# Performance work log

Measured on AMD Instinct MI355X. Metric: run time of the kernel, lower is better.

## Reference

```python
import jax, jax.numpy as jnp
import numpy as np
from jax.scipy.special import logsumexp

SINKHORN_ALPHA = 20.0
OT_MAX_ITER = 100
STOP_THR = 0.005


def setup_inputs() -> dict:
    key = jax.random.key(0)
    k1, k2 = jax.random.split(key)
    x = jax.random.normal(k1, (256, 384), dtype=jnp.float32)   # topic embeddings [K, D]
    y = jax.random.normal(k2, (32768, 384), dtype=jnp.float32)  # word embeddings  [V, D]
    return {"x": x, "y": y}


def reference(x, y):
    n, m = x.shape[0], y.shape[0]
    # FASTopic pairwise_euclidean_distance: squared euclidean cost [n, m]
    M = jnp.sum(x * x, axis=1, keepdims=True) + jnp.sum(y * y, axis=1) - 2.0 * (x @ y.T)
    a = jnp.full((n, 1), 1.0 / n, dtype=M.dtype)
    b = jnp.full((m, 1), 1.0 / m, dtype=M.dtype)
    log_a = jnp.log(a + 1e-30)
    log_b = jnp.log(b + 1e-30)
    log_K0 = -M * SINKHORN_ALPHA

    # State trick: the original mutates log_K only at the periodic absorption step
    # (log_K += log_u + log_v.T). We keep log_K = log_K0 + cum_u + cum_v.T so the
    # carried state is only O(n + m) vectors; math is identical.
    def body(state):
        log_u, log_v, cum_u, cum_v, err, cpt = state
        log_K = log_K0 + cum_u + cum_v.T                                    # [n, m]
        log_v_n = log_b - logsumexp(log_K.T + log_u.T, axis=1)[:, None]     # [m, 1]
        log_u_n = log_a - logsumexp(log_K + log_v_n.T, axis=1)[:, None]     # [n, 1]
        cpt_n = cpt + 1

        def absorb(_):
            cu = cum_u + log_u_n
            cv = cum_v + log_v_n
            lK = log_K0 + cu + cv.T
            # marginal check with log_u = log_v = 0 (matches check_convergence)
            row = jnp.exp(logsumexp(lK, axis=1))[:, None]
            col = jnp.exp(logsumexp(lK, axis=0))[:, None]
            e = jnp.maximum(jnp.max(jnp.abs(row - a)), jnp.max(jnp.abs(col - b)))
            return jnp.zeros_like(log_u_n), jnp.zeros_like(log_v_n), cu, cv, e

        def keep(_):
            return log_u_n, log_v_n, cum_u, cum_v, err

        lu, lv, cu, cv, e = jax.lax.cond(cpt_n % 50 == 1, absorb, keep, None)
        return (lu, lv, cu, cv, e, cpt_n)

    def cond_fn(state):
        err, cpt = state[4], state[5]
        return (err > STOP_THR) & (cpt < OT_MAX_ITER)

    init = (jnp.zeros((n, 1), M.dtype), jnp.zeros((m, 1), M.dtype),
            jnp.zeros((n, 1), M.dtype), jnp.zeros((m, 1), M.dtype),
            jnp.array(1.0, M.dtype), jnp.array(0, jnp.int32))
    log_u, log_v, cum_u, cum_v, _, _ = jax.lax.while_loop(cond_fn, body, init)

    log_K = log_K0 + cum_u + cum_v.T
    transp = jnp.exp(log_u) * (jnp.exp(log_K) * jnp.exp(log_v).T)  # diag(u) K diag(v)
    loss_ETP = jnp.sum(transp * M)
    return loss_ETP, transp
```

## Files before the change

### kernel.cpp

```cpp
#include <hip/hip_runtime.h>
#include <math.h>


#define N_TOPIC 256
#define N_WORD  32768

static constexpr float LOG_A = -5.545177444479562f;
static constexpr float LOG_B = -10.397207708399179f;
static constexpr float BVAL  = 3.0517578125e-05f;

typedef float f32x4 __attribute__((ext_vector_type(4)));
typedef short bf16x8 __attribute__((ext_vector_type(8)));

#define PIN4(v) asm volatile("" : "+v"((v).x), "+v"((v).y), "+v"((v).z), "+v"((v).w))

__global__ __launch_bounds__(256) void init_k(
    const float* __restrict__ x, const float* __restrict__ y,
    float* __restrict__ nx, float* __restrict__ ny, float* __restrict__ su,
    unsigned* __restrict__ colerr, int* __restrict__ active,
    int* __restrict__ counters, float* __restrict__ out)
{
    const int b = blockIdx.x, t = threadIdx.x;
    const int w = t >> 6, l = t & 63;
    if (b < 8192) {
        const int r = (b << 2) + w;
        const float4* y4 = (const float4*)y;
        float4 v = y4[r * 96 + l];
        float s = v.x * v.x + v.y * v.y + v.z * v.z + v.w * v.w;
        if (l < 32) {
            float4 u = y4[r * 96 + 64 + l];
            s += u.x * u.x + u.y * u.y + u.z * u.z + u.w * u.w;
        }
        for (int off = 32; off; off >>= 1) s += __shfl_down(s, off);
        if (l == 0) ny[r] = s;
    } else if (b < 8256) {
        const int r = ((b - 8192) << 2) + w;
        const float4* x4 = (const float4*)x;
        float4 v = x4[r * 96 + l];
        float s = v.x * v.x + v.y * v.y + v.z * v.z + v.w * v.w;
        if (l < 32) {
            float4 u = x4[r * 96 + 64 + l];
            s += u.x * u.x + u.y * u.y + u.z * u.z + u.w * u.w;
        }
        for (int off = 32; off; off >>= 1) s += __shfl_down(s, off);
        if (l == 0) { nx[r] = s; su[r] = -20.f * s; }
    } else {
        for (int k = t; k < 4096; k += 256) counters[k] = 0;
        if (t == 0) { colerr[0] = 0u; colerr[1] = 0u; active[0] = 1; out[0] = 0.f; }
    }
}

static __device__ __forceinline__ void split3(float v, ushort& h0, ushort& h1, ushort& h2)
{
    unsigned u0 = __float_as_uint(v);
    h0 = (ushort)(u0 >> 16);
    float r1 = v - __uint_as_float(u0 & 0xFFFF0000u);
    unsigned u1 = __float_as_uint(r1);
    h1 = (ushort)(u1 >> 16);
    float r2 = r1 - __uint_as_float(u1 & 0xFFFF0000u);
    h2 = (ushort)(__float_as_uint(r2) >> 16);
}

__global__ __launch_bounds__(256, 1) void gemm_k(
    const float* __restrict__ x, const float* __restrict__ y, float* __restrict__ G)
{
    __shared__ __align__(16) ushort xs0[5120], xs1[5120], xs2[5120];
    __shared__ __align__(16) ushort ys0[5120], ys1[5120], ys2[5120];

    const int t   = threadIdx.x;
    const int jb  = blockIdx.x << 7;
    const int ib  = blockIdx.y << 7;
    const int w   = t >> 6;
    const int ln  = t & 63;
    const int q   = ln >> 4;
    const int l15 = ln & 15;

    const float4* x4 = (const float4*)x;
    const float4* y4 = (const float4*)y;

    f32x4 acc[2][8];
#pragma unroll
    for (int mi = 0; mi < 2; ++mi)
#pragma unroll
        for (int nj = 0; nj < 8; ++nj) acc[mi][nj] = (f32x4){0.f, 0.f, 0.f, 0.f};

    for (int kc = 0; kc < 12; ++kc) {
        __syncthreads();
#pragma unroll
        for (int p = 0; p < 4; ++p) {
            const int f  = (t << 2) + p;
            const int r  = f >> 3, c4 = f & 7;
            const int o  = r * 40 + (c4 << 2);
            float4 vx = x4[(ib + r) * 96 + (kc << 3) + c4];
            ushort a0,a1,a2,b0,b1,b2,c0,c1,c2,d0,d1,d2;
            split3(vx.x, a0,a1,a2); split3(vx.y, b0,b1,b2);
            split3(vx.z, c0,c1,c2); split3(vx.w, d0,d1,d2);
            *(ushort4*)&xs0[o] = make_ushort4(a0,b0,c0,d0);
            *(ushort4*)&xs1[o] = make_ushort4(a1,b1,c1,d1);
            *(ushort4*)&xs2[o] = make_ushort4(a2,b2,c2,d2);
            float4 vy = y4[(jb + r) * 96 + (kc << 3) + c4];
            split3(vy.x, a0,a1,a2); split3(vy.y, b0,b1,b2);
            split3(vy.z, c0,c1,c2); split3(vy.w, d0,d1,d2);
            *(ushort4*)&ys0[o] = make_ushort4(a0,b0,c0,d0);
            *(ushort4*)&ys1[o] = make_ushort4(a1,b1,c1,d1);
            *(ushort4*)&ys2[o] = make_ushort4(a2,b2,c2,d2);
        }
        __syncthreads();

        bf16x8 A[3][2];
#pragma unroll
        for (int mi = 0; mi < 2; ++mi) {
            const int off = ((w << 5) + (mi << 4) + l15) * 40 + (q << 3);
            A[0][mi] = *(const bf16x8*)&xs0[off];
            A[1][mi] = *(const bf16x8*)&xs1[off];
            A[2][mi] = *(const bf16x8*)&xs2[off];
        }
#pragma unroll
        for (int nj = 0; nj < 8; ++nj) {
            const int off = ((nj << 4) + l15) * 40 + (q << 3);
            bf16x8 B0 = *(const bf16x8*)&ys0[off];
            bf16x8 B1 = *(const bf16x8*)&ys1[off];
            bf16x8 B2 = *(const bf16x8*)&ys2[off];
#pragma unroll
            for (int mi = 0; mi < 2; ++mi) {
                f32x4 c = acc[mi][nj];
                c = __builtin_amdgcn_mfma_f32_16x16x32_bf16(A[0][mi], B0, c, 0, 0, 0);
                c = __builtin_amdgcn_mfma_f32_16x16x32_bf16(A[0][mi], B1, c, 0, 0, 0);
                c = __builtin_amdgcn_mfma_f32_16x16x32_bf16(A[1][mi], B0, c, 0, 0, 0);
                c = __builtin_amdgcn_mfma_f32_16x16x32_bf16(A[1][mi], B1, c, 0, 0, 0);
                c = __builtin_amdgcn_mfma_f32_16x16x32_bf16(A[0][mi], B2, c, 0, 0, 0);
                c = __builtin_amdgcn_mfma_f32_16x16x32_bf16(A[2][mi], B0, c, 0, 0, 0);
                acc[mi][nj] = c;
            }
        }
    }
#pragma unroll
    for (int mi = 0; mi < 2; ++mi) {
        const int gi0 = ib + (w << 5) + (mi << 4) + (q << 2);
#pragma unroll
        for (int nj = 0; nj < 8; ++nj) {
            float* base = &G[(size_t)blockIdx.x * 32768 + (size_t)gi0 * 128
                             + (nj << 4) + l15];
#pragma unroll
            for (int r = 0; r < 4; ++r)
                base[r * 128] = 40.f * acc[mi][nj][r];
        }
    }
}

static __device__ __forceinline__ bool bar_arrive(int* cnt, int ph, int t, int* lastf)
{
    __threadfence();
    if (t == 0) *lastf = (atomicAdd(&cnt[ph], 1) == 255);
    __syncthreads();
    return *lastf != 0;
}
static __device__ __forceinline__ void bar_release(int* gen, int ph, int t)
{
    __threadfence();
    if (t == 0) atomicExch(gen, ph);
}
static __device__ __forceinline__ void bar_wait(int* gen, int ph, int t)
{
    if (t == 0) {
        while (atomicCAS(gen, -1, -1) < ph) __builtin_amdgcn_s_sleep(2);
    }
    __syncthreads();
    __threadfence();
}

__global__ __launch_bounds__(256, 1) void sink_loop(
    const float* __restrict__ G, float* __restrict__ su,
    float* __restrict__ W, float2* __restrict__ pms, float* __restrict__ prow,
    int* __restrict__ cnt, int* __restrict__ gen,
    unsigned* __restrict__ colerr, int* __restrict__ active)
{
    __shared__ float su_lds[256];
    __shared__ float mm[1024];
    __shared__ float ss[1024];
    __shared__ float Mcol[128];
    __shared__ float Wlds[128];
    __shared__ float ecol[128];
    __shared__ float Rlds[256];
    __shared__ float pq[256 * 33];
    __shared__ float errb[128];
    __shared__ int lastf;

    const int t  = threadIdx.x;
    const int b  = blockIdx.x;
    const int jq = t & 31;
    const int ig = t >> 5;
    const int c0 = jq << 2;
    int ph = 1;

    const float4* G4 = (const float4*)G;
    float4 tile[32];
#pragma unroll
    for (int k = 0; k < 32; ++k) {
        const int i = ig + (k << 3);
        tile[k] = G4[((size_t)b << 13) + (i << 5) + jq];
    }
#pragma unroll
    for (int k = 0; k < 32; ++k) PIN4(tile[k]);

    su_lds[t] = su[t];
    __syncthreads();

    {
        float m0=-INFINITY,m1=-INFINITY,m2=-INFINITY,m3=-INFINITY;
#pragma unroll
        for (int k = 0; k < 32; ++k) {
            const float sk = su_lds[ig + (k << 3)];
            m0=fmaxf(m0,tile[k].x+sk); m1=fmaxf(m1,tile[k].y+sk);
            m2=fmaxf(m2,tile[k].z+sk); m3=fmaxf(m3,tile[k].w+sk);
        }
        float s0=0.f,s1=0.f,s2=0.f,s3=0.f;
#pragma unroll
        for (int k = 0; k < 32; ++k) {
            const float sk = su_lds[ig + (k << 3)];
            s0+=__expf(tile[k].x+sk-m0); s1+=__expf(tile[k].y+sk-m1);
            s2+=__expf(tile[k].z+sk-m2); s3+=__expf(tile[k].w+sk-m3);
        }
        mm[ig*128+c0+0]=m0; ss[ig*128+c0+0]=s0;
        mm[ig*128+c0+1]=m1; ss[ig*128+c0+1]=s1;
        mm[ig*128+c0+2]=m2; ss[ig*128+c0+2]=s2;
        mm[ig*128+c0+3]=m3; ss[ig*128+c0+3]=s3;
        __syncthreads();
        if (t < 128) {
            float m=-INFINITY, s=0.f;
#pragma unroll
            for (int q = 0; q < 8; ++q) {
                float pmv=mm[q*128+t], psv=ss[q*128+t];
                float nm=fmaxf(m,pmv);
                s = s*__expf(m-nm) + psv*__expf(pmv-nm);
                m = nm;
            }
            Wlds[t] = LOG_B - (m + __logf(s));
        }
        __syncthreads();
    }
    {
#pragma unroll
        for (int k = 0; k < 32; ++k) {
            const int i = ig + (k << 3);
            float a0=tile[k].x+Wlds[c0], a1=tile[k].y+Wlds[c0+1];
            float a2=tile[k].z+Wlds[c0+2], a3=tile[k].w+Wlds[c0+3];
            pq[i*33+jq] = fmaxf(fmaxf(a0,a1), fmaxf(a2,a3));
        }
        __syncthreads();
        {
            float R=-INFINITY;
#pragma unroll
            for (int q = 0; q < 32; ++q) R = fmaxf(R, pq[t*33+q]);
            Rlds[t] = R;
        }
        __syncthreads();
#pragma unroll
        for (int k = 0; k < 32; ++k) {
            const int i = ig + (k << 3);
            const float Rr = Rlds[i];
            float s = __expf(tile[k].x+Wlds[c0]-Rr)   + __expf(tile[k].y+Wlds[c0+1]-Rr)
                    + __expf(tile[k].z+Wlds[c0+2]-Rr) + __expf(tile[k].w+Wlds[c0+3]-Rr);
            pq[i*33+jq] = s;
        }
        __syncthreads();
        {
            float s = 0.f;
#pragma unroll
            for (int q = 0; q < 32; ++q) s += pq[t*33+q];
            pms[(b << 8) + t] = make_float2(Rlds[t], s);
        }
    }
    if (bar_arrive(cnt, ph, t, &lastf)) {
        __threadfence();
        float m=-INFINITY, s=0.f;
        for (int p = 0; p < 256; ++p) {
            float2 v = pms[(p << 8) + t];
            float nm = fmaxf(m, v.x);
            s = s*__expf(m-nm) + v.y*__expf(v.x-nm);
            m = nm;
        }
        su[t] = LOG_A - (m + __logf(s));
        bar_release(gen, ph, t);
    }
    bar_wait(gen, ph, t); ++ph;
    su_lds[t] = su[t];
    __syncthreads();

    int act;
    {
        float m0=-INFINITY,m1=-INFINITY,m2=-INFINITY,m3=-INFINITY;
#pragma unroll
        for (int k = 0; k < 32; ++k) {
            const float sk = su_lds[ig + (k << 3)];
            m0=fmaxf(m0,tile[k].x+sk); m1=fmaxf(m1,tile[k].y+sk);
            m2=fmaxf(m2,tile[k].z+sk); m3=fmaxf(m3,tile[k].w+sk);
        }
        float s0=0.f,s1=0.f,s2=0.f,s3=0.f;
#pragma unroll
        for (int k = 0; k < 32; ++k) {
            const float sk = su_lds[ig + (k << 3)];
            s0+=__expf(tile[k].x+sk-m0); s1+=__expf(tile[k].y+sk-m1);
            s2+=__expf(tile[k].z+sk-m2); s3+=__expf(tile[k].w+sk-m3);
        }
        mm[ig*128+c0+0]=m0; ss[ig*128+c0+0]=s0;
        mm[ig*128+c0+1]=m1; ss[ig*128+c0+1]=s1;
        mm[ig*128+c0+2]=m2; ss[ig*128+c0+2]=s2;
        mm[ig*128+c0+3]=m3; ss[ig*128+c0+3]=s3;
        __syncthreads();
        float d = 0.f;
        if (t < 128) {
            float m=-INFINITY, s=0.f;
#pragma unroll
            for (int q = 0; q < 8; ++q) {
                float pmv=mm[q*128+t], psv=ss[q*128+t];
                float nm=fmaxf(m,pmv);
                s = s*__expf(m-nm) + psv*__expf(pmv-nm);
                m = nm;
            }
            d = fabsf(__expf((m + __logf(s)) + Wlds[t]) - BVAL);
            errb[t] = d;
        }
        __syncthreads();
        for (int n = 64; n; n >>= 1) {
            if (t < n) errb[t] = fmaxf(errb[t], errb[t + n]);
            __syncthreads();
        }
        if (t == 0) atomicMax(&colerr[0], __float_as_uint(errb[0]));
        if (bar_arrive(cnt, ph, t, &lastf)) {
            if (t == 0) {
                unsigned e = atomicMax(&colerr[0], 0u);
                active[0] = (__uint_as_float(e) > 0.005f) ? 1 : 0;
            }
            bar_release(gen, ph, t);
        }
        bar_wait(gen, ph, t); ++ph;
        act = active[0];
    }

    if (act) {
#pragma unroll 1
        for (int tt = 2; tt <= 100; ++tt) {
            {
                float m0=-INFINITY,m1=-INFINITY,m2=-INFINITY,m3=-INFINITY;
#pragma unroll
                for (int k = 0; k < 32; ++k) {
                    const float sk = su_lds[ig + (k << 3)];
                    m0=fmaxf(m0,tile[k].x+sk); m1=fmaxf(m1,tile[k].y+sk);
                    m2=fmaxf(m2,tile[k].z+sk); m3=fmaxf(m3,tile[k].w+sk);
                }
                mm[ig*128+c0+0]=m0; mm[ig*128+c0+1]=m1;
                mm[ig*128+c0+2]=m2; mm[ig*128+c0+3]=m3;
                __syncthreads();
                if (t < 128) {
                    float m=-INFINITY;
#pragma unroll
                    for (int q = 0; q < 8; ++q) m = fmaxf(m, mm[q*128+t]);
                    Mcol[t] = m;
                }
                __syncthreads();
            }
            float4 E[32];
            {
                const float Mc0=Mcol[c0], Mc1=Mcol[c0+1], Mc2=Mcol[c0+2], Mc3=Mcol[c0+3];
                float s0=0.f,s1=0.f,s2=0.f,s3=0.f;
#pragma unroll
                for (int k = 0; k < 32; ++k) {
                    const float sk = su_lds[ig + (k << 3)];
                    E[k].x=__expf(tile[k].x+sk-Mc0); s0+=E[k].x;
                    E[k].y=__expf(tile[k].y+sk-Mc1); s1+=E[k].y;
                    E[k].z=__expf(tile[k].z+sk-Mc2); s2+=E[k].z;
                    E[k].w=__expf(tile[k].w+sk-Mc3); s3+=E[k].w;
                }
                ss[ig*128+c0+0]=s0; ss[ig*128+c0+1]=s1;
                ss[ig*128+c0+2]=s2; ss[ig*128+c0+3]=s3;
                __syncthreads();
                if (t < 128) {
                    float ssum = 0.f;
#pragma unroll
                    for (int q = 0; q < 8; ++q) ssum += ss[q*128+t];
                    Wlds[t] = LOG_B - (Mcol[t] + __logf(ssum));
                    ecol[t] = 1.0f / ssum;
                }
                __syncthreads();
            }
            {
                const float e0=ecol[c0], e1=ecol[c0+1], e2=ecol[c0+2], e3=ecol[c0+3];
#pragma unroll
                for (int k = 0; k < 32; ++k) {
                    const int i = ig + (k << 3);
                    pq[i*33+jq] = E[k].x*e0 + E[k].y*e1 + E[k].z*e2 + E[k].w*e3;
                }
                __syncthreads();
                float s = 0.f;
#pragma unroll
                for (int q = 0; q < 32; ++q) s += pq[t*33+q];
                prow[(b << 8) + t] = s;
            }
            if (bar_arrive(cnt, ph, t, &lastf)) {
                __threadfence();
                float tot = 0.f;
                for (int p = 0; p < 256; ++p) tot += prow[(p << 8) + t];
                su[t] = (LOG_A - LOG_B) + su_lds[t] - __logf(tot);
                bar_release(gen, ph, t);
            }
            bar_wait(gen, ph, t); ++ph;
            su_lds[t] = su[t];
            __syncthreads();

            if (tt == 51) {
                float m0=-INFINITY,m1=-INFINITY,m2=-INFINITY,m3=-INFINITY;
#pragma unroll
                for (int k = 0; k < 32; ++k) {
                    const float sk = su_lds[ig + (k << 3)];
                    m0=fmaxf(m0,tile[k].x+sk); m1=fmaxf(m1,tile[k].y+sk);
                    m2=fmaxf(m2,tile[k].z+sk); m3=fmaxf(m3,tile[k].w+sk);
                }
                float s0=0.f,s1=0.f,s2=0.f,s3=0.f;
#pragma unroll
                for (int k = 0; k < 32; ++k) {
                    const float sk = su_lds[ig + (k << 3)];
                    s0+=__expf(tile[k].x+sk-m0); s1+=__expf(tile[k].y+sk-m1);
                    s2+=__expf(tile[k].z+sk-m2); s3+=__expf(tile[k].w+sk-m3);
                }
                mm[ig*128+c0+0]=m0; ss[ig*128+c0+0]=s0;
                mm[ig*128+c0+1]=m1; ss[ig*128+c0+1]=s1;
                mm[ig*128+c0+2]=m2; ss[ig*128+c0+2]=s2;
                mm[ig*128+c0+3]=m3; ss[ig*128+c0+3]=s3;
                __syncthreads();
                if (t < 128) {
                    float m=-INFINITY, s=0.f;
#pragma unroll
                    for (int q = 0; q < 8; ++q) {
                        float pmv=mm[q*128+t], psv=ss[q*128+t];
                        float nm=fmaxf(m,pmv);
                        s = s*__expf(m-nm) + psv*__expf(pmv-nm);
                        m = nm;
                    }
                    errb[t] = fabsf(__expf((m + __logf(s)) + Wlds[t]) - BVAL);
                }
                __syncthreads();
                for (int n = 64; n; n >>= 1) {
                    if (t < n) errb[t] = fmaxf(errb[t], errb[t + n]);
                    __syncthreads();
                }
                if (t == 0) atomicMax(&colerr[1], __float_as_uint(errb[0]));
                if (bar_arrive(cnt, ph, t, &lastf)) {
                    if (t == 0) {
                        unsigned e = atomicMax(&colerr[1], 0u);
                        active[0] = (__uint_as_float(e) > 0.005f) ? 1 : 0;
                    }
                    bar_release(gen, ph, t);
                }
                bar_wait(gen, ph, t); ++ph;
                if (active[0] == 0) break;
            }
        }
    }

    if (t < 128) W[(b << 7) + t] = Wlds[t];
}

__global__ __launch_bounds__(256) void finalize_k(
    const float* __restrict__ G, const float* __restrict__ su,
    const float* __restrict__ W, const float* __restrict__ nx,
    const float* __restrict__ ny, float* __restrict__ out)
{
    __shared__ float su_lds[256], nx_lds[256];
    __shared__ float red[4];
    const int t = threadIdx.x, b = blockIdx.x;
    const int j0 = b << 7;
    const int jq = t & 31;
    const int ig = t >> 5;
    su_lds[t] = su[t];
    nx_lds[t] = nx[t];
    __syncthreads();

    const float4* G4 = (const float4*)G;
    const float4 Wq  = ((const float4*)W)[(j0 >> 2) + jq];
    const float4 nyq = ((const float4*)ny)[(j0 >> 2) + jq];
    const int jbase = 1 + j0 + (jq << 2);
    float acc = 0.f;
#pragma unroll 4
    for (int it = 0; it < 32; ++it) {
        const int i = ig + (it << 3);
        float4 g = G4[((size_t)b << 13) + (i << 5) + jq];
        const float si = su_lds[i], nxi = nx_lds[i];
        float v0 = __expf(g.x + si + Wq.x);
        float v1 = __expf(g.y + si + Wq.y);
        float v2 = __expf(g.z + si + Wq.z);
        float v3 = __expf(g.w + si + Wq.w);
        float* o = out + jbase + (size_t)i * 32768;
        __builtin_nontemporal_store(v0, o + 0);
        __builtin_nontemporal_store(v1, o + 1);
        __builtin_nontemporal_store(v2, o + 2);
        __builtin_nontemporal_store(v3, o + 3);
        acc += v0 * (nxi + nyq.x - 0.05f * g.x) +
               v1 * (nxi + nyq.y - 0.05f * g.y) +
               v2 * (nxi + nyq.z - 0.05f * g.z) +
               v3 * (nxi + nyq.w - 0.05f * g.w);
    }
    for (int off = 32; off; off >>= 1) acc += __shfl_down(acc, off);
    if ((t & 63) == 0) red[t >> 6] = acc;
    __syncthreads();
    if (t == 0) atomicAdd(out, red[0] + red[1] + red[2] + red[3]);
}

extern "C" void kernel_launch(void* const* d_in, const int* in_sizes, int n_in,
                              void* d_out, int out_size, void* d_ws, size_t ws_size,
                              hipStream_t stream)
{
    const float* x = (const float*)d_in[0];
    const float* y = (const float*)d_in[1];
    float* out = (float*)d_out;

    float* ws   = (float*)d_ws;
    float* G    = ws;
    float* Wv   = G + 8388608;
    float* su   = Wv + 32768;
    float* nx   = su + 256;
    float* ny   = nx + 256;
    float2* pms = (float2*)(ny + 32768);
    float* prow = (float*)(pms + 65536);
    unsigned* colerr = (unsigned*)(prow + 65536);
    int* active   = (int*)(colerr + 2);
    int* counters = active + 1;
    int* gen      = counters + 3000;

    init_k<<<8257, 256, 0, stream>>>(x, y, nx, ny, su, colerr, active, counters, out);
    gemm_k<<<dim3(256, 2), 256, 0, stream>>>(x, y, G);
    sink_loop<<<256, 256, 0, stream>>>(G, su, Wv, pms, prow,
                                       counters, gen, colerr, active);
    finalize_k<<<256, 256, 0, stream>>>(G, su, Wv, nx, ny, out);
}
```

Baseline: 308.2 us.

## Fuse GEMM, Sinkhorn loop and finalize into one persistent kernel

Merges the GEMM, the persistent Sinkhorn loop and the finalize kernel into a single 256-block kernel. Each block computes its own 256x128 cost tile in MFMA registers, moves it into the register tile through LDS, and reuses that tile for the final transport-plan output. This removes the 32 MB G write and its two reads, plus two kernel launches. In exchange each block now does the whole GEMM for its column strip (x split into bf16 parts per block, 4x8 accumulators), which means only 256 blocks run the GEMM and register pressure rises.

```diff
diff --git a/kernel.cpp b/kernel.cpp
--- a/kernel.cpp
+++ b/kernel.cpp
@@ -61,59 +61,110 @@
     h2 = (ushort)(__float_as_uint(r2) >> 16);
 }
 
-__global__ __launch_bounds__(256, 1) void gemm_k(
-    const float* __restrict__ x, const float* __restrict__ y, float* __restrict__ G)
-{
-    __shared__ __align__(16) ushort xs0[5120], xs1[5120], xs2[5120];
-    __shared__ __align__(16) ushort ys0[5120], ys1[5120], ys2[5120];
-
-    const int t   = threadIdx.x;
-    const int jb  = blockIdx.x << 7;
-    const int ib  = blockIdx.y << 7;
-    const int w   = t >> 6;
-    const int ln  = t & 63;
-    const int q   = ln >> 4;
-    const int l15 = ln & 15;
+static __device__ __forceinline__ bool bar_arrive(int* cnt, int ph, int t, int* lastf)
+{
+    __threadfence();
+    if (t == 0) *lastf = (atomicAdd(&cnt[ph], 1) == 255);
+    __syncthreads();
+    return *lastf != 0;
+}
+static __device__ __forceinline__ void bar_release(int* gen, int ph, int t)
+{
+    __threadfence();
+    if (t == 0) atomicExch(gen, ph);
+}
+static __device__ __forceinline__ void bar_wait(int* gen, int ph, int t)
+{
+    if (t == 0) {
+        while (atomicCAS(gen, -1, -1) < ph) __builtin_amdgcn_s_sleep(2);
+    }
+    __syncthreads();
+    __threadfence();
+}
+
+__global__ __launch_bounds__(256, 1) void fused_k(
+    const float* __restrict__ x, const float* __restrict__ y,
+    float* __restrict__ su, const float* __restrict__ nx,
+    const float* __restrict__ ny, float2* __restrict__ pms,
+    float* __restrict__ prow, int* __restrict__ cnt, int* __restrict__ gen,
+    unsigned* __restrict__ colerr, int* __restrict__ active,
+    float* __restrict__ out)
+{
+    __shared__ __align__(16) char smem[63488];
+    __shared__ int lastf;
+    float4* xs4 = (float4*)smem;
+    ushort* ys0 = (ushort*)(smem + 32768);
+    ushort* ys1 = (ushort*)(smem + 43008);
+    ushort* ys2 = (ushort*)(smem + 53248);
+    float* su_lds = (float*)smem;
+    float* mm    = (float*)(smem + 1024);
+    float* ss    = (float*)(smem + 5120);
+    float* Mcol  = (float*)(smem + 9216);
+    float* Wlds  = (float*)(smem + 9728);
+    float* ecol  = (float*)(smem + 10240);
+    float* Rlds  = (float*)(smem + 10752);
+    float* errb  = (float*)(smem + 11776);
+    float* nxl   = (float*)(smem + 12288);
+    float* nyl   = (float*)(smem + 13312);
+    float* pq    = (float*)(smem + 13824);
+    float* cv    = pq;
+
+    const int t  = threadIdx.x;
+    const int b  = blockIdx.x;
+    const int w  = t >> 6, ln = t & 63, q = ln >> 4, l15 = ln & 15;
+    const int jq = t & 31, ig = t >> 5, c0 = jq << 2;
+    const int jy0 = b << 7;
+    int ph = 1;
 
     const float4* x4 = (const float4*)x;
     const float4* y4 = (const float4*)y;
 
-    f32x4 acc[2][8];
-#pragma unroll
-    for (int mi = 0; mi < 2; ++mi)
+    f32x4 acc[4][8];
+#pragma unroll
+    for (int mi = 0; mi < 4; ++mi)
 #pragma unroll
         for (int nj = 0; nj < 8; ++nj) acc[mi][nj] = (f32x4){0.f, 0.f, 0.f, 0.f};
 
     for (int kc = 0; kc < 12; ++kc) {
         __syncthreads();
 #pragma unroll
+        for (int p = 0; p < 8; ++p) {
+            const int f = (p << 8) + t;
+            const int r = f >> 3, c4 = f & 7;
+            xs4[(r << 3) + (c4 ^ (r & 7))] = x4[r * 96 + (kc << 3) + c4];
+        }
+#pragma unroll
         for (int p = 0; p < 4; ++p) {
-            const int f  = (t << 2) + p;
-            const int r  = f >> 3, c4 = f & 7;
-            const int o  = r * 40 + (c4 << 2);
-            float4 vx = x4[(ib + r) * 96 + (kc << 3) + c4];
-            ushort a0,a1,a2,b0,b1,b2,c0,c1,c2,d0,d1,d2;
-            split3(vx.x, a0,a1,a2); split3(vx.y, b0,b1,b2);
-            split3(vx.z, c0,c1,c2); split3(vx.w, d0,d1,d2);
-            *(ushort4*)&xs0[o] = make_ushort4(a0,b0,c0,d0);
-            *(ushort4*)&xs1[o] = make_ushort4(a1,b1,c1,d1);
-            *(ushort4*)&xs2[o] = make_ushort4(a2,b2,c2,d2);
-            float4 vy = y4[(jb + r) * 96 + (kc << 3) + c4];
+            const int f = (p << 8) + t;
+            const int r = f >> 3, c4 = f & 7;
+            float4 vy = y4[(size_t)(jy0 + r) * 96 + (kc << 3) + c4];
+            ushort a0,a1,a2,b0,b1,b2,g0,g1,g2,d0,d1,d2;
             split3(vy.x, a0,a1,a2); split3(vy.y, b0,b1,b2);
-            split3(vy.z, c0,c1,c2); split3(vy.w, d0,d1,d2);
-            *(ushort4*)&ys0[o] = make_ushort4(a0,b0,c0,d0);
-            *(ushort4*)&ys1[o] = make_ushort4(a1,b1,c1,d1);
-            *(ushort4*)&ys2[o] = make_ushort4(a2,b2,c2,d2);
-        }
-        __syncthreads();
-
-        bf16x8 A[3][2];
-#pragma unroll
-        for (int mi = 0; mi < 2; ++mi) {
-            const int off = ((w << 5) + (mi << 4) + l15) * 40 + (q << 3);
-            A[0][mi] = *(const bf16x8*)&xs0[off];
-            A[1][mi] = *(const bf16x8*)&xs1[off];
-            A[2][mi] = *(const bf16x8*)&xs2[off];
+            split3(vy.z, g0,g1,g2); split3(vy.w, d0,d1,d2);
+            *(ushort4*)&ys0[r * 40 + (c4 << 2)] = make_ushort4(a0,b0,g0,d0);
+            *(ushort4*)&ys1[r * 40 + (c4 << 2)] = make_ushort4(a1,b1,g1,d1);
+            *(ushort4*)&ys2[r * 40 + (c4 << 2)] = make_ushort4(a2,b2,g2,d2);
+        }
+        __syncthreads();
+
+        union U8 { ushort u[8]; bf16x8 v; };
+        bf16x8 A0[4], A1[4], A2[4];
+#pragma unroll
+        for (int mi = 0; mi < 4; ++mi) {
+            const int row = (w << 6) + (mi << 4) + l15;
+            const int base = row << 3;
+            float4 xa = xs4[base + (((q << 1) + 0) ^ (row & 7))];
+            float4 xb = xs4[base + (((q << 1) + 1) ^ (row & 7))];
+            U8 u0, u1, u2;
+            split3(xa.x, u0.u[0], u1.u[0], u2.u[0]);
+            split3(xa.y, u0.u[1], u1.u[1], u2.u[1]);
+            split3(xa.z, u0.u[2], u1.u[2], u2.u[2]);
+            split3(xa.w, u0.u[3], u1.u[3], u2.u[3]);
+            split3(xb.x, u0.u[4], u1.u[4], u2.u[4]);
+            split3(xb.y, u0.u[5], u1.u[5], u2.u[5]);
+            split3(xb.z, u0.u[6], u1.u[6], u2.u[6]);
+            split3(xb.w, u0.u[7], u1.u[7], u2.u[7]);
+            A0[mi] = u0.v; A1[mi] = u1.v; A2[mi] = u2.v;
         }
 #pragma unroll
         for (int nj = 0; nj < 8; ++nj) {
@@ -122,87 +173,47 @@
             bf16x8 B1 = *(const bf16x8*)&ys1[off];
             bf16x8 B2 = *(const bf16x8*)&ys2[off];
 #pragma unroll
-            for (int mi = 0; mi < 2; ++mi) {
+            for (int mi = 0; mi < 4; ++mi) {
                 f32x4 c = acc[mi][nj];
-                c = __builtin_amdgcn_mfma_f32_16x16x32_bf16(A[0][mi], B0, c, 0, 0, 0);
-                c = __builtin_amdgcn_mfma_f32_16x16x32_bf16(A[0][mi], B1, c, 0, 0, 0);
-                c = __builtin_amdgcn_mfma_f32_16x16x32_bf16(A[1][mi], B0, c, 0, 0, 0);
-                c = __builtin_amdgcn_mfma_f32_16x16x32_bf16(A[1][mi], B1, c, 0, 0, 0);
-                c = __builtin_amdgcn_mfma_f32_16x16x32_bf16(A[0][mi], B2, c, 0, 0, 0);
-                c = __builtin_amdgcn_mfma_f32_16x16x32_bf16(A[2][mi], B0, c, 0, 0, 0);
+                c = __builtin_amdgcn_mfma_f32_16x16x32_bf16(A0[mi], B0, c, 0, 0, 0);
+                c = __builtin_amdgcn_mfma_f32_16x16x32_bf16(A0[mi], B1, c, 0, 0, 0);
+                c = __builtin_amdgcn_mfma_f32_16x16x32_bf16(A1[mi], B0, c, 0, 0, 0);
+                c = __builtin_amdgcn_mfma_f32_16x16x32_bf16(A1[mi], B1, c, 0, 0, 0);
+                c = __builtin_amdgcn_mfma_f32_16x16x32_bf16(A0[mi], B2, c, 0, 0, 0);
+                c = __builtin_amdgcn_mfma_f32_16x16x32_bf16(A2[mi], B0, c, 0, 0, 0);
                 acc[mi][nj] = c;
             }
         }
     }
-#pragma unroll
-    for (int mi = 0; mi < 2; ++mi) {
-        const int gi0 = ib + (w << 5) + (mi << 4) + (q << 2);
-#pragma unroll
-        for (int nj = 0; nj < 8; ++nj) {
-            float* base = &G[(size_t)blockIdx.x * 32768 + (size_t)gi0 * 128
-                             + (nj << 4) + l15];
-#pragma unroll
-            for (int r = 0; r < 4; ++r)
-                base[r * 128] = 40.f * acc[mi][nj][r];
-        }
-    }
-}
-
-static __device__ __forceinline__ bool bar_arrive(int* cnt, int ph, int t, int* lastf)
-{
-    __threadfence();
-    if (t == 0) *lastf = (atomicAdd(&cnt[ph], 1) == 255);
-    __syncthreads();
-    return *lastf != 0;
-}
-static __device__ __forceinline__ void bar_release(int* gen, int ph, int t)
-{
-    __threadfence();
-    if (t == 0) atomicExch(gen, ph);
-}
-static __device__ __forceinline__ void bar_wait(int* gen, int ph, int t)
-{
-    if (t == 0) {
-        while (atomicCAS(gen, -1, -1) < ph) __builtin_amdgcn_s_sleep(2);
-    }
-    __syncthreads();
-    __threadfence();
-}
-
-__global__ __launch_bounds__(256, 1) void sink_loop(
-    const float* __restrict__ G, float* __restrict__ su,
-    float* __restrict__ W, float2* __restrict__ pms, float* __restrict__ prow,
-    int* __restrict__ cnt, int* __restrict__ gen,
-    unsigned* __restrict__ colerr, int* __restrict__ active)
-{
-    __shared__ float su_lds[256];
-    __shared__ float mm[1024];
-    __shared__ float ss[1024];
-    __shared__ float Mcol[128];
-    __shared__ float Wlds[128];
-    __shared__ float ecol[128];
-    __shared__ float Rlds[256];
-    __shared__ float pq[256 * 33];
-    __shared__ float errb[128];
-    __shared__ int lastf;
-
-    const int t  = threadIdx.x;
-    const int b  = blockIdx.x;
-    const int jq = t & 31;
-    const int ig = t >> 5;
-    const int c0 = jq << 2;
-    int ph = 1;
-
-    const float4* G4 = (const float4*)G;
+
     float4 tile[32];
 #pragma unroll
-    for (int k = 0; k < 32; ++k) {
-        const int i = ig + (k << 3);
-        tile[k] = G4[((size_t)b << 13) + (i << 5) + jq];
+    for (int c = 0; c < 4; ++c) {
+        __syncthreads();
+        if (w == c) {
+#pragma unroll
+            for (int mi = 0; mi < 4; ++mi) {
+                const int rl = (mi << 4) + (q << 2);
+#pragma unroll
+                for (int nj = 0; nj < 8; ++nj) {
+                    const int col = (nj << 4) + l15;
+#pragma unroll
+                    for (int r = 0; r < 4; ++r)
+                        cv[(rl + r) * 132 + col] = 40.f * acc[mi][nj][r];
+                }
+            }
+        }
+        __syncthreads();
+#pragma unroll
+        for (int kk = 0; kk < 8; ++kk) {
+            const int il = ig + (kk << 3);
+            tile[(c << 3) + kk] = *(const float4*)&cv[il * 132 + c0];
+        }
     }
 #pragma unroll
     for (int k = 0; k < 32; ++k) PIN4(tile[k]);
 
+    __syncthreads();
     su_lds[t] = su[t];
     __syncthreads();
 
@@ -229,8 +240,8 @@
         if (t < 128) {
             float m=-INFINITY, s=0.f;
 #pragma unroll
-            for (int q = 0; q < 8; ++q) {
-                float pmv=mm[q*128+t], psv=ss[q*128+t];
+            for (int qq = 0; qq < 8; ++qq) {
+                float pmv=mm[qq*128+t], psv=ss[qq*128+t];
                 float nm=fmaxf(m,pmv);
                 s = s*__expf(m-nm) + psv*__expf(pmv-nm);
                 m = nm;
@@ -251,7 +262,7 @@
         {
             float R=-INFINITY;
 #pragma unroll
-            for (int q = 0; q < 32; ++q) R = fmaxf(R, pq[t*33+q]);
+            for (int qq = 0; qq < 32; ++qq) R = fmaxf(R, pq[t*33+qq]);
             Rlds[t] = R;
         }
         __syncthreads();
@@ -267,7 +278,7 @@
         {
             float s = 0.f;
 #pragma unroll
-            for (int q = 0; q < 32; ++q) s += pq[t*33+q];
+            for (int qq = 0; qq < 32; ++qq) s += pq[t*33+qq];
             pms[(b << 8) + t] = make_float2(Rlds[t], s);
         }
     }
@@ -308,18 +319,16 @@
         mm[ig*128+c0+2]=m2; ss[ig*128+c0+2]=s2;
         mm[ig*128+c0+3]=m3; ss[ig*128+c0+3]=s3;
         __syncthreads();
-        float d = 0.f;
         if (t < 128) {
             float m=-INFINITY, s=0.f;
 #pragma unroll
-            for (int q = 0; q < 8; ++q) {
-                float pmv=mm[q*128+t], psv=ss[q*128+t];
+            for (int qq = 0; qq < 8; ++qq) {
+                float pmv=mm[qq*128+t], psv=ss[qq*128+t];
                 float nm=fmaxf(m,pmv);
                 s = s*__expf(m-nm) + psv*__expf(pmv-nm);
                 m = nm;
             }
-            d = fabsf(__expf((m + __logf(s)) + Wlds[t]) - BVAL);
-            errb[t] = d;
+            errb[t] = fabsf(__expf((m + __logf(s)) + Wlds[t]) - BVAL);
         }
         __syncthreads();
         for (int n = 64; n; n >>= 1) {
@@ -355,7 +364,7 @@
                 if (t < 128) {
                     float m=-INFINITY;
 #pragma unroll
-                    for (int q = 0; q < 8; ++q) m = fmaxf(m, mm[q*128+t]);
+                    for (int qq = 0; qq < 8; ++qq) m = fmaxf(m, mm[qq*128+t]);
                     Mcol[t] = m;
                 }
                 __syncthreads();
@@ -378,7 +387,7 @@
                 if (t < 128) {
                     float ssum = 0.f;
 #pragma unroll
-                    for (int q = 0; q < 8; ++q) ssum += ss[q*128+t];
+                    for (int qq = 0; qq < 8; ++qq) ssum += ss[qq*128+t];
                     Wlds[t] = LOG_B - (Mcol[t] + __logf(ssum));
                     ecol[t] = 1.0f / ssum;
                 }
@@ -394,7 +403,7 @@
                 __syncthreads();
                 float s = 0.f;
 #pragma unroll
-                for (int q = 0; q < 32; ++q) s += pq[t*33+q];
+                for (int qq = 0; qq < 32; ++qq) s += pq[t*33+qq];
                 prow[(b << 8) + t] = s;
             }
             if (bar_arrive(cnt, ph, t, &lastf)) {
@@ -431,8 +440,8 @@
                 if (t < 128) {
                     float m=-INFINITY, s=0.f;
 #pragma unroll
-                    for (int q = 0; q < 8; ++q) {
-                        float pmv=mm[q*128+t], psv=ss[q*128+t];
+                    for (int qq = 0; qq < 8; ++qq) {
+                        float pmv=mm[qq*128+t], psv=ss[qq*128+t];
                         float nm=fmaxf(m,pmv);
                         s = s*__expf(m-nm) + psv*__expf(pmv-nm);
                         m = nm;
@@ -458,52 +467,34 @@
         }
     }
 
-    if (t < 128) W[(b << 7) + t] = Wlds[t];
-}
-
-__global__ __launch_bounds__(256) void finalize_k(
-    const float* __restrict__ G, const float* __restrict__ su,
-    const float* __restrict__ W, const float* __restrict__ nx,
-    const float* __restrict__ ny, float* __restrict__ out)
-{
-    __shared__ float su_lds[256], nx_lds[256];
-    __shared__ float red[4];
-    const int t = threadIdx.x, b = blockIdx.x;
-    const int j0 = b << 7;
-    const int jq = t & 31;
-    const int ig = t >> 5;
-    su_lds[t] = su[t];
-    nx_lds[t] = nx[t];
-    __syncthreads();
-
-    const float4* G4 = (const float4*)G;
-    const float4 Wq  = ((const float4*)W)[(j0 >> 2) + jq];
-    const float4 nyq = ((const float4*)ny)[(j0 >> 2) + jq];
-    const int jbase = 1 + j0 + (jq << 2);
-    float acc = 0.f;
+    nxl[t] = nx[t];
+    if (t < 128) nyl[t] = ny[jy0 + t];
+    __syncthreads();
+
+    float accl = 0.f;
 #pragma unroll 4
-    for (int it = 0; it < 32; ++it) {
-        const int i = ig + (it << 3);
-        float4 g = G4[((size_t)b << 13) + (i << 5) + jq];
-        const float si = su_lds[i], nxi = nx_lds[i];
-        float v0 = __expf(g.x + si + Wq.x);
-        float v1 = __expf(g.y + si + Wq.y);
-        float v2 = __expf(g.z + si + Wq.z);
-        float v3 = __expf(g.w + si + Wq.w);
-        float* o = out + jbase + (size_t)i * 32768;
+    for (int k = 0; k < 32; ++k) {
+        const int i = ig + (k << 3);
+        const float si = su_lds[i], nxi = nxl[i];
+        const float g0 = tile[k].x, g1 = tile[k].y, g2 = tile[k].z, g3 = tile[k].w;
+        float v0 = __expf(g0 + si + Wlds[c0+0]);
+        float v1 = __expf(g1 + si + Wlds[c0+1]);
+        float v2 = __expf(g2 + si + Wlds[c0+2]);
+        float v3 = __expf(g3 + si + Wlds[c0+3]);
+        float* o = out + 1 + (size_t)i * 32768 + jy0 + c0;
         __builtin_nontemporal_store(v0, o + 0);
         __builtin_nontemporal_store(v1, o + 1);
         __builtin_nontemporal_store(v2, o + 2);
         __builtin_nontemporal_store(v3, o + 3);
-        acc += v0 * (nxi + nyq.x - 0.05f * g.x) +
-               v1 * (nxi + nyq.y - 0.05f * g.y) +
-               v2 * (nxi + nyq.z - 0.05f * g.z) +
-               v3 * (nxi + nyq.w - 0.05f * g.w);
-    }
-    for (int off = 32; off; off >>= 1) acc += __shfl_down(acc, off);
-    if ((t & 63) == 0) red[t >> 6] = acc;
-    __syncthreads();
-    if (t == 0) atomicAdd(out, red[0] + red[1] + red[2] + red[3]);
+        accl += v0 * (nxi + nyl[c0+0] - 0.05f * g0) +
+                v1 * (nxi + nyl[c0+1] - 0.05f * g1) +
+                v2 * (nxi + nyl[c0+2] - 0.05f * g2) +
+                v3 * (nxi + nyl[c0+3] - 0.05f * g3);
+    }
+    for (int off = 32; off; off >>= 1) accl += __shfl_down(accl, off);
+    if (ln == 0) errb[w] = accl;
+    __syncthreads();
+    if (t == 0) atomicAdd(out, errb[0] + errb[1] + errb[2] + errb[3]);
 }
 
 extern "C" void kernel_launch(void* const* d_in, const int* in_sizes, int n_in,
@@ -515,9 +506,7 @@
     float* out = (float*)d_out;
 
     float* ws   = (float*)d_ws;
-    float* G    = ws;
-    float* Wv   = G + 8388608;
-    float* su   = Wv + 32768;
+    float* su   = ws;
     float* nx   = su + 256;
     float* ny   = nx + 256;
     float2* pms = (float2*)(ny + 32768);
@@ -528,8 +517,6 @@
     int* gen      = counters + 3000;
 
     init_k<<<8257, 256, 0, stream>>>(x, y, nx, ny, su, colerr, active, counters, out);
-    gemm_k<<<dim3(256, 2), 256, 0, stream>>>(x, y, G);
-    sink_loop<<<256, 256, 0, stream>>>(G, su, Wv, pms, prow,
-                                       counters, gen, colerr, active);
-    finalize_k<<<256, 256, 0, stream>>>(G, su, Wv, nx, ny, out);
-}
+    fused_k<<<256, 256, 0, stream>>>(x, y, su, nx, ny, pms, prow,
+                                     counters, gen, colerr, active, out);
+}
```

Result: slower. 326.3 us (+5.9%).
